# Kernel tuning notes

Hardware: AMD Instinct MI355X
Metric: run time of the kernel (lower is better)

Reference implementation:

```python
import jax, jax.numpy as jnp
import numpy as np
import math

# ---- module hyperparameters (from init_kwargs) ----
N = 3            # polynomial points per segment
SEGMENTS = 512   # piecewise segments over [-1, 1] (length = 2.0)
ROTATIONS = 4    # -> 2*ROTATIONS stripe directions
WIDTH = 512
HEIGHT = 512
MAX_DIM = max(WIDTH, HEIGHT)
RATIO = MAX_DIM / (MAX_DIM + 1)
NUM_POS = 2 * ROTATIONS
NW = SEGMENTS * (N - 1) + 1  # continuous piecewise weights per channel

# Chebyshev-Lobatto interpolation points on [-1, 1]
CHEB = (-np.cos(np.pi * np.arange(N) / (N - 1))).astype(np.float32)


def make_positions():
    """Rotated stripe position maps, [2*ROTATIONS, WIDTH, HEIGHT], precomputed buffers."""
    xv, yv = np.meshgrid(np.arange(WIDTH), np.arange(HEIGHT), indexing='ij')
    xv = xv.astype(np.float32)
    yv = yv.astype(np.float32)
    pos = []
    for i in range(ROTATIONS):
        theta = math.pi / 2.0 * (i / ROTATIONS)
        cx, cy = math.cos(theta), math.sin(theta)
        for sgn in (1.0, -1.0):  # r1 = cx*x + cy*y, r2 = cx*x - cy*y
            r = cx * xv + sgn * cy * yv
            rmin, rmax = r.min(), r.max()
            dr = rmax - rmin
            r = ((r - rmin) * RATIO / dr - 0.5) * MAX_DIM
            pos.append(r)
    return np.stack(pos, 0).astype(np.float32)


POSITIONS = jnp.asarray(make_positions())  # [8, W, H] constant buffer


def lagrange_basis(t):
    """Lagrange basis at Chebyshev-Lobatto points; t [...], returns [..., N]."""
    bs = []
    for k in range(N):
        b = jnp.ones_like(t)
        for j in range(N):
            if j != k:
                b = b * (t - CHEB[j]) / (CHEB[k] - CHEB[j])
        bs.append(b)
    return jnp.stack(bs, axis=-1)


def piecewise_shared(xin, w):
    """Continuous piecewise Lagrange polynomial, weights shared across positions.
    xin: [B, C, L] in ~[-1, 1]; w: [C, NW]. Returns [B, C, L]."""
    xs = (xin + 1.0) * (0.5 * SEGMENTS)              # segment-space coordinate
    sid = jnp.clip(jnp.floor(xs), 0.0, SEGMENTS - 1)  # segment index (clamped)
    t = 2.0 * (xs - sid) - 1.0                        # local coord in [-1, 1]
    sid = sid.astype(jnp.int32)
    widx = sid[..., None] * (N - 1) + jnp.arange(N)   # [B, C, L, N] weight gather idx
    cidx = jnp.arange(w.shape[0])[None, :, None, None]
    wg = w[cidx, widx]                                # [B, C, L, N]
    return jnp.sum(lagrange_basis(t) * wg, axis=-1)


def setup_inputs() -> dict:
    key = jax.random.key(0)
    k1, k2 = jax.random.split(key)
    x = jax.random.normal(k1, (16, 3, WIDTH, HEIGHT), dtype=jnp.float32)
    weights = jax.random.normal(k2, (NUM_POS, 3, NW), dtype=jnp.float32)  # weight_magnitude=1
    return {"x": x, "weights": weights}


def reference(x, weights):
    B, C, W, H = x.shape
    accum = jnp.zeros((B, C, W * H), dtype=x.dtype)
    for i in range(NUM_POS):
        # position_encode: pixel value perturbs its stripe position, then rescale to [-1,1]
        dl = (0.5 * x + POSITIONS[i]) / (0.5 * MAX_DIM)  # [B, C, W, H]
        dl = dl.reshape(B, C, W * H)
        accum = accum + piecewise_shared(dl, weights[i])
    accum = accum / NUM_POS
    return accum.reshape(x.shape)
```

## Files before the change

kernel.cpp:

```cpp
#include <hip/hip_runtime.h>
#include <math.h>


#define WDIM 512
#define HDIM 512
#define SEGS 512
#define NPOS 8
#define NW   1025
#define CCH  3

#define THREADS 256
#define PIX_PER_THREAD 16
#define PIX_PER_BLOCK (THREADS * PIX_PER_THREAD)
#define CHUNKS ((WDIM * HDIM) / PIX_PER_BLOCK)

struct Params {
    float ax[NPOS];
    float ay[NPOS];
    float c0[NPOS];
};

union HalfPack {
    unsigned int u;
    _Float16 h[2];
};

__global__ __launch_bounds__(THREADS, 5)
void stripe_poly_kernel(const float* __restrict__ x,
                        const float* __restrict__ w,
                        float* __restrict__ out,
                        Params P)
{
    __shared__ uint2 lut[NPOS][SEGS];

    const int slice = blockIdx.x / CHUNKS;
    const int chunk = blockIdx.x % CHUNKS;
    const int ch    = slice % CCH;

    for (int idx = threadIdx.x; idx < NPOS * SEGS; idx += THREADS) {
        const int p = idx >> 9;
        const int s = idx & (SEGS - 1);
        const float* wp = w + ((size_t)p * CCH + ch) * NW + 2 * s;
        const float w0 = wp[0], w1 = wp[1], w2 = wp[2];
        const float c1 = 0.5f * (w2 - w0);
        const float c2 = fmaf(0.5f, w0 + w2, -w1);
        HalfPack hp;
        hp.h[0] = (_Float16)c1;
        hp.h[1] = (_Float16)c2;
        lut[p][s] = make_uint2(__float_as_uint(w1), hp.u);
    }
    __syncthreads();

    const size_t slice_off = (size_t)slice * (WDIM * HDIM);
    const int base = chunk * PIX_PER_BLOCK;

    for (int k = 0; k < PIX_PER_THREAD / 4; ++k) {
        const int p0 = base + ((k * THREADS + threadIdx.x) << 2);
        const float4 xin = *(const float4*)(x + slice_off + p0);
        const float xf = (float)(p0 >> 9);
        const float yf = (float)(p0 & (HDIM - 1));
        const float xv[4] = {xin.x, xin.y, xin.z, xin.w};
        float acc[4] = {0.f, 0.f, 0.f, 0.f};

        #pragma unroll
        for (int i = 0; i < NPOS; ++i) {
            const float ay = P.ay[i];
            const float g  = fmaf(ay, yf, fmaf(P.ax[i], xf, P.c0[i]));
            #pragma unroll
            for (int j = 0; j < 4; ++j) {
                const float xs = fmaf(0.5f, xv[j], fmaf(ay, (float)j, g));
                float sf = floorf(xs);
                sf = fminf(fmaxf(sf, 0.0f), (float)(SEGS - 1));
                const int s = (int)sf;
                const float t = fmaf(2.0f, xs - sf, -1.0f);
                const uint2 v = lut[i][s];
                HalfPack hp; hp.u = v.y;
                const float c0 = __uint_as_float(v.x);
                const float c1 = (float)hp.h[0];
                const float c2 = (float)hp.h[1];
                acc[j] += c0 + t * fmaf(t, c2, c1);
            }
        }

        float4 o;
        o.x = acc[0] * 0.125f;
        o.y = acc[1] * 0.125f;
        o.z = acc[2] * 0.125f;
        o.w = acc[3] * 0.125f;
        *(float4*)(out + slice_off + p0) = o;
    }
}

extern "C" void kernel_launch(void* const* d_in, const int* in_sizes, int n_in,
                              void* d_out, int out_size, void* d_ws, size_t ws_size,
                              hipStream_t stream)
{
    const float* x = (const float*)d_in[0];
    const float* w = (const float*)d_in[1];
    float* out = (float*)d_out;

    Params P;
    const double ratio_f = (double)(float)(512.0 / 513.0);
    for (int i = 0; i < 4; ++i) {
        const double theta = (M_PI * 0.5) * ((double)i / 4.0);
        const float a   = (float)cos(theta);
        const float cyf = (float)sin(theta);
        for (int sg = 0; sg < 2; ++sg) {
            const float b = (sg == 0) ? cyf : -cyf;
            const float ax511 = a * 511.0f;
            const float by511 = b * 511.0f;
            float rmin, rmax;
            if (sg == 0) { rmin = 0.0f;  rmax = ax511 + by511; }
            else         { rmin = by511; rmax = ax511; }
            const float dr = rmax - rmin;
            const double K = 512.0 * ratio_f / (double)dr;
            const int pi = 2 * i + sg;
            P.ax[pi] = (float)(K * (double)a);
            P.ay[pi] = (float)(K * (double)b);
            P.c0[pi] = (float)(-K * (double)rmin);
        }
    }

    const int slices = in_sizes[0] / (WDIM * HDIM);
    const int blocks = slices * CHUNKS;
    stripe_poly_kernel<<<blocks, THREADS, 0, stream>>>(x, w, out, P);
}
```

Measured before the change: 134.2 us.

## Merge identical position maps into one table and use 2D tiles for LDS locality

Positions 0 and 1 (theta=0, both signs) give the same stripe coordinate, so their weights are summed into a single table. That cuts the inner loop from 8 to 7 lookups per pixel. The 1/8 averaging is folded into the LUT coefficients and the accumulate becomes FMAs. Blocks now cover 64x64 2D tiles with 512 threads instead of linear row chunks, so lanes in a wavefront hit nearby segments in the LDS table. The risk is fp16 rounding differences, since scaled and summed coefficients are stored in half precision.

```diff
diff --git a/kernel.cpp b/kernel.cpp
--- a/kernel.cpp
+++ b/kernel.cpp
@@ -6,13 +6,13 @@
 #define HDIM 512
 #define SEGS 512
 #define NPOS 8
+#define NTAB 7
 #define NW   1025
 #define CCH  3
 
-#define THREADS 256
-#define PIX_PER_THREAD 16
-#define PIX_PER_BLOCK (THREADS * PIX_PER_THREAD)
-#define CHUNKS ((WDIM * HDIM) / PIX_PER_BLOCK)
+#define THREADS 512
+#define TILE 64
+#define TILES_PER_SLICE ((WDIM / TILE) * (HDIM / TILE))
 
 struct Params {
     float ax[NPOS];
@@ -25,47 +25,67 @@
     _Float16 h[2];
 };
 
-__global__ __launch_bounds__(THREADS, 5)
+__global__ __launch_bounds__(THREADS, 8)
 void stripe_poly_kernel(const float* __restrict__ x,
                         const float* __restrict__ w,
                         float* __restrict__ out,
                         Params P)
 {
-    __shared__ uint2 lut[NPOS][SEGS];
+    __shared__ uint2 lut[NTAB][SEGS];
 
-    const int slice = blockIdx.x / CHUNKS;
-    const int chunk = blockIdx.x % CHUNKS;
+    const int slice = blockIdx.x / TILES_PER_SLICE;
+    const int tile  = blockIdx.x % TILES_PER_SLICE;
     const int ch    = slice % CCH;
+    const int bx    = (tile >> 3) * TILE;
+    const int by    = (tile & 7) * TILE;
 
-    for (int idx = threadIdx.x; idx < NPOS * SEGS; idx += THREADS) {
-        const int p = idx >> 9;
+    for (int idx = threadIdx.x; idx < NTAB * SEGS; idx += THREADS) {
+        const int m = idx >> 9;
         const int s = idx & (SEGS - 1);
-        const float* wp = w + ((size_t)p * CCH + ch) * NW + 2 * s;
-        const float w0 = wp[0], w1 = wp[1], w2 = wp[2];
-        const float c1 = 0.5f * (w2 - w0);
-        const float c2 = fmaf(0.5f, w0 + w2, -w1);
+        float w0, w1, w2;
+        if (m == 0) {
+            const float* wa = w + (size_t)(0 * CCH + ch) * NW + 2 * s;
+            const float* wb = w + (size_t)(1 * CCH + ch) * NW + 2 * s;
+            w0 = wa[0] + wb[0]; w1 = wa[1] + wb[1]; w2 = wa[2] + wb[2];
+        } else {
+            const float* wp = w + (size_t)((m + 1) * CCH + ch) * NW + 2 * s;
+            w0 = wp[0]; w1 = wp[1]; w2 = wp[2];
+        }
+        const float c0 = 0.125f * w1;
+        const float c1 = 0.0625f * (w2 - w0);
+        const float c2 = 0.125f * fmaf(0.5f, w0 + w2, -w1);
         HalfPack hp;
         hp.h[0] = (_Float16)c1;
         hp.h[1] = (_Float16)c2;
-        lut[p][s] = make_uint2(__float_as_uint(w1), hp.u);
+        lut[m][s] = make_uint2(__float_as_uint(c0), hp.u);
     }
     __syncthreads();
 
+    const int tid  = threadIdx.x;
+    const int wv   = tid >> 6;
+    const int lane = tid & 63;
+    const int px_w = (wv >> 2) * 16;
+    const int py_w = (wv & 3) * 16;
+    const int px_l = lane >> 2;
+    const int py_l = (lane & 3) * 4;
+
     const size_t slice_off = (size_t)slice * (WDIM * HDIM);
-    const int base = chunk * PIX_PER_BLOCK;
+    const int py = by + py_w + py_l;
+    const float yf = (float)py;
 
-    for (int k = 0; k < PIX_PER_THREAD / 4; ++k) {
-        const int p0 = base + ((k * THREADS + threadIdx.x) << 2);
-        const float4 xin = *(const float4*)(x + slice_off + p0);
-        const float xf = (float)(p0 >> 9);
-        const float yf = (float)(p0 & (HDIM - 1));
+    for (int k = 0; k < 2; ++k) {
+        const int px = bx + px_w + k * 32 + px_l;
+        const size_t p0 = slice_off + (size_t)px * HDIM + py;
+        const float4 xin = *(const float4*)(x + p0);
+        const float xf = (float)px;
         const float xv[4] = {xin.x, xin.y, xin.z, xin.w};
         float acc[4] = {0.f, 0.f, 0.f, 0.f};
 
         #pragma unroll
-        for (int i = 0; i < NPOS; ++i) {
-            const float ay = P.ay[i];
-            const float g  = fmaf(ay, yf, fmaf(P.ax[i], xf, P.c0[i]));
+        for (int i = 0; i < NTAB; ++i) {
+            const int pi = (i == 0) ? 0 : (i + 1);
+            const float ay = P.ay[pi];
+            const float g  = fmaf(ay, yf, fmaf(P.ax[pi], xf, P.c0[pi]));
             #pragma unroll
             for (int j = 0; j < 4; ++j) {
                 const float xs = fmaf(0.5f, xv[j], fmaf(ay, (float)j, g));
@@ -75,19 +95,14 @@
                 const float t = fmaf(2.0f, xs - sf, -1.0f);
                 const uint2 v = lut[i][s];
                 HalfPack hp; hp.u = v.y;
-                const float c0 = __uint_as_float(v.x);
-                const float c1 = (float)hp.h[0];
-                const float c2 = (float)hp.h[1];
-                acc[j] += c0 + t * fmaf(t, c2, c1);
+                const float u = fmaf(t, (float)hp.h[1], (float)hp.h[0]);
+                acc[j] = fmaf(t, u, acc[j] + __uint_as_float(v.x));
             }
         }
 
         float4 o;
-        o.x = acc[0] * 0.125f;
-        o.y = acc[1] * 0.125f;
-        o.z = acc[2] * 0.125f;
-        o.w = acc[3] * 0.125f;
-        *(float4*)(out + slice_off + p0) = o;
+        o.x = acc[0]; o.y = acc[1]; o.z = acc[2]; o.w = acc[3];
+        *(float4*)(out + p0) = o;
     }
 }
 
@@ -122,6 +137,6 @@
     }
 
     const int slices = in_sizes[0] / (WDIM * HDIM);
-    const int blocks = slices * CHUNKS;
+    const int blocks = slices * TILES_PER_SLICE;
     stripe_poly_kernel<<<blocks, THREADS, 0, stream>>>(x, w, out, P);
 }
```

Result: faster. 117.3 us (-12.6%).
